# Kernel tuning notes

Hardware: AMD Instinct MI355X
Metric: run time of the kernel (lower is better)

## Reference

```python
import jax, jax.numpy as jnp
import numpy as np

EPS = 1e-05

def _rms_norm(x, w, eps=EPS):
    xf = x.astype(jnp.float32)
    var = jnp.mean(xf * xf, axis=-1, keepdims=True)
    return (x * jax.lax.rsqrt(var + eps)) * w

def _apply_rotary_emb(x, freqs_cis):
    # x: [B,S,H,D], freqs_cis: [B,S,D] with cos in first half, sin in second
    half = freqs_cis.shape[-1] // 2
    cos = freqs_cis[..., :half][:, :, None, :]  # [B,S,1,D/2]
    sin = freqs_cis[..., half:][:, :, None, :]
    xf = x.astype(jnp.float32).reshape(*x.shape[:-1], -1, 2)
    xr, xi = xf[..., 0], xf[..., 1]
    out_r = xr * cos - xi * sin
    out_i = xr * sin + xi * cos
    out = jnp.stack([out_r, out_i], axis=-1).reshape(x.shape)
    return out.astype(x.dtype)

def setup_inputs() -> dict:
    key = jax.random.key(0)
    ks = jax.random.split(key, 8)
    B, S, D, H = 2, 4096, 2048, 16
    hd = D // H
    scale = 1.0 / np.sqrt(D)
    x = jax.random.normal(ks[0], (B, S, D), dtype=jnp.float32)
    freqs_cis = jax.random.normal(ks[1], (B, S, hd), dtype=jnp.float32)
    wq = jax.random.normal(ks[2], (D, D), dtype=jnp.float32) * scale
    wk = jax.random.normal(ks[3], (D, D), dtype=jnp.float32) * scale
    wv = jax.random.normal(ks[4], (D, D), dtype=jnp.float32) * scale
    wo = jax.random.normal(ks[5], (D, D), dtype=jnp.float32) * scale
    norm_q_w = jnp.ones((hd,), dtype=jnp.float32)
    norm_k_w = jnp.ones((hd,), dtype=jnp.float32)
    return {"x": x, "freqs_cis": freqs_cis, "wq": wq, "wk": wk, "wv": wv,
            "wo": wo, "norm_q_w": norm_q_w, "norm_k_w": norm_k_w}

def reference(x, freqs_cis, wq, wk, wv, wo, norm_q_w, norm_k_w):
    B, S, D = x.shape
    H = 16
    hd = D // H
    # Linear with torch convention: y = x @ W^T
    q = (x @ wq.T).reshape(B, S, H, hd)
    k = (x @ wk.T).reshape(B, S, H, hd)
    v = (x @ wv.T).reshape(B, S, H, hd)
    q = _rms_norm(q, norm_q_w)
    k = _rms_norm(k, norm_k_w)
    q = _apply_rotary_emb(q, freqs_cis)
    k = _apply_rotary_emb(k, freqs_cis)
    # SDPA: [B,H,S,hd]
    scale = 1.0 / jnp.sqrt(jnp.asarray(hd, dtype=jnp.float32))
    scores = jnp.einsum('bqhd,bkhd->bhqk', q, k) * scale
    attn = jax.nn.softmax(scores, axis=-1)
    out = jnp.einsum('bhqk,bkhd->bqhd', attn, v).reshape(B, S, D)
    return out @ wo.T
```

## Files before the change

kernel.cpp:

```cpp
#include <hip/hip_runtime.h>
#include <hip/hip_bf16.h>
#include <cstdint>
#include <cstdio>

typedef unsigned short ushort_t;
typedef __attribute__((ext_vector_type(8))) __bf16 bf16x8;
typedef __attribute__((ext_vector_type(2))) __bf16 bhalf2_t;
typedef __attribute__((ext_vector_type(8))) unsigned short us8;
typedef __attribute__((ext_vector_type(4))) unsigned short us4;
typedef __attribute__((ext_vector_type(4))) float f32x4;
typedef __attribute__((ext_vector_type(2))) float f32x2;

__device__ __forceinline__ ushort_t f2b(float f) {
  uint32_t u = __builtin_bit_cast(uint32_t, f);
  uint32_t r = (u + 0x7fffu + ((u >> 16) & 1u)) >> 16;
  return (ushort_t)r;
}
__device__ __forceinline__ float b2f(ushort_t s) {
  return __builtin_bit_cast(float, (uint32_t)s << 16);
}

__device__ __forceinline__ void gld_lds16(const void* g, void* l) {
  __builtin_amdgcn_global_load_lds(
      (__attribute__((address_space(1))) void*)(uintptr_t)g,
      (__attribute__((address_space(3))) void*)(uint32_t)(uintptr_t)l,
      16, 0, 0);
}

__global__ void cast_f2b(const float* __restrict__ src, ushort_t* __restrict__ dst, int n4) {
  int i = blockIdx.x * 256 + threadIdx.x;
  if (i < n4) {
    float4 f = ((const float4*)src)[i];
    us4 o = { f2b(f.x), f2b(f.y), f2b(f.z), f2b(f.w) };
    ((us4*)dst)[i] = o;
  }
}

__global__ void cast3_f2b(const float* __restrict__ a, const float* __restrict__ b,
                          const float* __restrict__ c, ushort_t* __restrict__ dst) {
  int i = blockIdx.x * 256 + threadIdx.x;
  int seg = i >> 20, local = i & 1048575;
  const float* src = (seg == 0) ? a : (seg == 1) ? b : c;
  float4 f = ((const float4*)src)[local];
  us4 o = { f2b(f.x), f2b(f.y), f2b(f.z), f2b(f.w) };
  ((us4*)dst)[i] = o;
}

template <typename OutT>
__global__ __launch_bounds__(256, 3) void gemm_bt(const ushort_t* __restrict__ A,
                                                  const ushort_t* __restrict__ B,
                                                  OutT* __restrict__ C,
                                                  int M, int N, int K) {
  __shared__ ushort_t As[128 * 64];
  __shared__ ushort_t Bs[128 * 64];
  const int w    = threadIdx.x >> 6;
  const int lane = threadIdx.x & 63;
  const int m_l  = lane & 15;
  const int quad = lane >> 4;
  const int m0 = blockIdx.y * 128, n0 = blockIdx.x * 128;
  const int wr = (w >> 1) * 64, wc = (w & 1) * 64;

  f32x4 acc[4][4];
#pragma unroll
  for (int i = 0; i < 4; ++i)
#pragma unroll
    for (int j = 0; j < 4; ++j) acc[i][j] = (f32x4){0.f, 0.f, 0.f, 0.f};

  const int lr = lane >> 3;
  const int sc8 = ((lane & 7) ^ lr) * 8;

  for (int k0 = 0; k0 < K; k0 += 64) {
#pragma unroll
    for (int t = 0; t < 4; ++t) {
      int ra = w * 32 + t * 8;
      gld_lds16(A + (size_t)(m0 + ra + lr) * K + k0 + sc8, &As[ra * 64]);
      gld_lds16(B + (size_t)(n0 + ra + lr) * K + k0 + sc8, &Bs[ra * 64]);
    }
    __syncthreads();
#pragma unroll
    for (int kk = 0; kk < 2; ++kk) {
      bf16x8 af[4], bf[4];
#pragma unroll
      for (int mt = 0; mt < 4; ++mt) {
        int row = wr + mt * 16 + m_l;
        af[mt] = __builtin_bit_cast(bf16x8,
            *(const us8*)&As[row * 64 + ((kk * 4 + quad) ^ (m_l & 7)) * 8]);
      }
#pragma unroll
      for (int nt = 0; nt < 4; ++nt) {
        int row = wc + nt * 16 + m_l;
        bf[nt] = __builtin_bit_cast(bf16x8,
            *(const us8*)&Bs[row * 64 + ((kk * 4 + quad) ^ (m_l & 7)) * 8]);
      }
#pragma unroll
      for (int mt = 0; mt < 4; ++mt)
#pragma unroll
        for (int nt = 0; nt < 4; ++nt)
          acc[mt][nt] = __builtin_amdgcn_mfma_f32_16x16x32_bf16(af[mt], bf[nt], acc[mt][nt], 0, 0, 0);
    }
    __syncthreads();
  }
#pragma unroll
  for (int mt = 0; mt < 4; ++mt)
#pragma unroll
    for (int nt = 0; nt < 4; ++nt)
#pragma unroll
      for (int r = 0; r < 4; ++r) {
        int row = m0 + wr + mt * 16 + quad * 4 + r;
        int col = n0 + wc + nt * 16 + m_l;
        float v = acc[mt][nt][r];
        if constexpr (__is_same(OutT, float)) C[(size_t)row * N + col] = v;
        else                                  C[(size_t)row * N + col] = f2b(v);
      }
}

__global__ void rmsrope(ushort_t* __restrict__ qkv, const float* __restrict__ freqs,
                        const float* __restrict__ wq, const float* __restrict__ wk) {
  int w = threadIdx.x >> 6, lane = threadIdx.x & 63;
  int rid = blockIdx.x * 4 + w;
  int h = rid & 15;
  int m = (rid >> 4) & 8191;
  int qk = rid >> 17;
  ushort_t* row = qkv + (size_t)m * 6144 + qk * 2048 + h * 128;
  uint32_t pr = *(const uint32_t*)(row + 2 * lane);
  float xr = b2f((ushort_t)(pr & 0xffff));
  float xi = b2f((ushort_t)(pr >> 16));
  float ss = xr * xr + xi * xi;
#pragma unroll
  for (int o = 1; o < 64; o <<= 1) ss += __shfl_xor(ss, o);
  float rinv = rsqrtf(ss * (1.f / 128.f) + 1e-5f);
  const float* wn = qk ? wk : wq;
  float nr = xr * rinv * wn[2 * lane];
  float ni = xi * rinv * wn[2 * lane + 1];
  float fc = freqs[(size_t)m * 128 + lane];
  float fs = freqs[(size_t)m * 128 + 64 + lane];
  float orr = nr * fc - ni * fs;
  float oii = nr * fs + ni * fc;
  const float k1 = 0.08838834764831845f * 1.4426950408889634f;
  float fscale = (qk == 0) ? k1 : 1.0f;
  orr *= fscale;
  oii *= fscale;
  *(uint32_t*)(row + 2 * lane) = (uint32_t)f2b(orr) | ((uint32_t)f2b(oii) << 16);
}

__global__ void transpose_v(const ushort_t* __restrict__ qkv, ushort_t* __restrict__ vt) {
  __shared__ ushort_t tile[64][136];
  int bh = blockIdx.y, s0 = blockIdx.x * 64;
  int b = bh >> 4, h = bh & 15;
  const ushort_t* src = qkv + (size_t)(b * 4096 + s0) * 6144 + 4096 + h * 128;
  int t = threadIdx.x;
  int r = t >> 2, c0 = (t & 3) * 32;
#pragma unroll
  for (int j = 0; j < 4; ++j)
    *(us8*)&tile[r][c0 + 8 * j] = *(const us8*)(src + (size_t)r * 6144 + c0 + 8 * j);
  __syncthreads();
  int d = t >> 1, sh = (t & 1) * 32;
  ushort_t* dst = vt + (size_t)bh * 524288 + (size_t)d * 4096 + s0 + sh;
#pragma unroll
  for (int i0 = 0; i0 < 32; i0 += 8) {
    us8 o;
#pragma unroll
    for (int j = 0; j < 8; ++j) o[j] = tile[sh + i0 + j][d];
    *(us8*)(dst + i0) = o;
  }
}

__global__ __launch_bounds__(256, 3) void flash_attn(const ushort_t* __restrict__ qkv,
                                                     const ushort_t* __restrict__ vt,
                                                     ushort_t* __restrict__ op0,
                                                     ushort_t* __restrict__ op1,
                                                     ushort_t* __restrict__ op2,
                                                     ushort_t* __restrict__ lbase) {
  __shared__ ushort_t Ks[64 * 128];
  __shared__ ushort_t VTs[128 * 64];

  const int w = threadIdx.x >> 6, lane = threadIdx.x & 63;
  const int m_l = lane & 15, quad = lane >> 4;

  const int id = blockIdx.x;
  const int xcd = id & 7, j = id >> 3;
  const int combo = xcd * 12 + (j >> 5);
  const int q0 = (j & 31) * 128;
  const int bh = combo & 31, split = combo >> 5;
  const int b = bh >> 4, h = bh & 15;
  const int kvbeg = split * 1344;
  const int kvend = (split == 2) ? 4096 : kvbeg + 1344;
  ushort_t* op = (split == 0) ? op0 : (split == 1) ? op1 : op2;

  const ushort_t* qb = qkv + (size_t)(b * 4096 + q0) * 6144 + h * 128;
  const ushort_t* kb = qkv + (size_t)(b * 4096) * 6144 + 2048 + h * 128;
  const ushort_t* vb = vt + (size_t)bh * 524288;

  const int lr = lane >> 4, p15 = lane & 15;

  bf16x8 qf[2][4];
  const int rowq = w * 16 + m_l;
  const int sqr = (m_l & 3) | ((m_l >> 3) << 2) | ((w & 1) << 3);
#pragma unroll
  for (int g = 0; g < 2; ++g) {
    __syncthreads();
#pragma unroll
    for (int t = 0; t < 4; ++t) {
      int rbase = w * 16 + t * 4;
      int sst = lr | ((t >> 1) << 2) | ((w & 1) << 3);
      gld_lds16(qb + (size_t)(g * 64 + rbase + lr) * 6144 + (p15 ^ sst) * 8, &Ks[rbase * 128]);
    }
    __syncthreads();
#pragma unroll
    for (int kk = 0; kk < 4; ++kk)
      qf[g][kk] = __builtin_bit_cast(bf16x8,
          *(const us8*)&Ks[rowq * 128 + ((kk * 4 + quad) ^ sqr) * 8]);
  }

  int kbase[4];
#pragma unroll
  for (int mt = 0; mt < 4; ++mt)
    kbase[mt] = ((m_l >> 2) * 8 + (m_l & 3) + (mt & 1) * 4 + (mt >> 1) * 32) * 128;
  int cx[4];
#pragma unroll
  for (int kk = 0; kk < 4; ++kk) cx[kk] = ((kk * 4 + quad) ^ m_l) * 8;
  int vx[2];
#pragma unroll
  for (int kk = 0; kk < 2; ++kk) vx[kk] = ((kk * 4 + quad) ^ (m_l & 7)) * 8;

  f32x4 lacc[2] = {(f32x4){0.f, 0.f, 0.f, 0.f}, (f32x4){0.f, 0.f, 0.f, 0.f}};
  f32x4 Oa[2][8];
#pragma unroll
  for (int g = 0; g < 2; ++g)
#pragma unroll
    for (int nt = 0; nt < 8; ++nt) Oa[g][nt] = (f32x4){0.f, 0.f, 0.f, 0.f};

  for (int kv0 = kvbeg; kv0 < kvend; kv0 += 64) {
    __syncthreads();
    {
#pragma unroll
      for (int t = 0; t < 4; ++t) {
        int rbase = w * 16 + t * 4;
        int sst = lr | ((t >> 1) << 2) | ((w & 1) << 3);
        gld_lds16(kb + (size_t)(kv0 + rbase + lr) * 6144 + (p15 ^ sst) * 8, &Ks[rbase * 128]);
      }
      int lr2 = lane >> 3, s2 = (lane & 7) ^ lr2;
#pragma unroll
      for (int t = 0; t < 4; ++t) {
        int r = w * 32 + t * 8;
        gld_lds16(vb + (size_t)(r + lr2) * 4096 + kv0 + s2 * 8, &VTs[r * 64]);
      }
    }
    __syncthreads();

    f32x4 S[2][4];
#pragma unroll
    for (int g = 0; g < 2; ++g)
#pragma unroll
      for (int mt = 0; mt < 4; ++mt) S[g][mt] = (f32x4){0.f, 0.f, 0.f, 0.f};
#pragma unroll
    for (int kk = 0; kk < 4; ++kk)
#pragma unroll
      for (int mt = 0; mt < 4; ++mt) {
        bf16x8 kf = __builtin_bit_cast(bf16x8, *(const us8*)&Ks[kbase[mt] + cx[kk]]);
        S[0][mt] = __builtin_amdgcn_mfma_f32_16x16x32_bf16(kf, qf[0][kk], S[0][mt], 0, 0, 0);
        S[1][mt] = __builtin_amdgcn_mfma_f32_16x16x32_bf16(kf, qf[1][kk], S[1][mt], 0, 0, 0);
      }

    union Upf { us8 u; bhalf2_t h[4]; } pf[2][2];
#pragma unroll
    for (int g = 0; g < 2; ++g) {
      f32x4 pe[4];
#pragma unroll
      for (int mt = 0; mt < 4; ++mt)
#pragma unroll
        for (int r = 0; r < 4; ++r)
          pe[mt][r] = __builtin_amdgcn_exp2f(S[g][mt][r]);
      lacc[g] += (pe[0] + pe[1]) + (pe[2] + pe[3]);
#pragma unroll
      for (int kk = 0; kk < 2; ++kk)
#pragma unroll
        for (int t = 0; t < 4; ++t) {
          int mt = kk * 2 + (t >> 1), r0 = (t & 1) * 2;
          f32x2 a = { pe[mt][r0], pe[mt][r0 + 1] };
          pf[g][kk].h[t] = __builtin_convertvector(a, bhalf2_t);
        }
    }

#pragma unroll
    for (int kk = 0; kk < 2; ++kk) {
      bf16x8 p0 = __builtin_bit_cast(bf16x8, pf[0][kk].u);
      bf16x8 p1 = __builtin_bit_cast(bf16x8, pf[1][kk].u);
#pragma unroll
      for (int nt = 0; nt < 8; ++nt) {
        bf16x8 vf = __builtin_bit_cast(bf16x8,
            *(const us8*)&VTs[(nt * 16 + m_l) * 64 + vx[kk]]);
        Oa[0][nt] = __builtin_amdgcn_mfma_f32_16x16x32_bf16(p0, vf, Oa[0][nt], 0, 0, 0);
        Oa[1][nt] = __builtin_amdgcn_mfma_f32_16x16x32_bf16(p1, vf, Oa[1][nt], 0, 0, 0);
      }
    }
  }

#pragma unroll
  for (int g = 0; g < 2; ++g) {
    float lsum = (lacc[g][0] + lacc[g][1]) + (lacc[g][2] + lacc[g][3]);
    lsum += __shfl_xor(lsum, 16);
    lsum += __shfl_xor(lsum, 32);
    if (quad == 0) {
      int s = q0 + g * 64 + w * 16 + m_l;
      *(float*)(lbase + (size_t)(b * 4096 + s) * 6144 + 4096 + h * 128 + split * 2) = lsum;
    }
#pragma unroll
    for (int r = 0; r < 4; ++r) {
      int s = q0 + g * 64 + w * 16 + quad * 4 + r;
      ushort_t* dst = op + (size_t)(b * 4096 + s) * 2048 + h * 128;
#pragma unroll
      for (int nt = 0; nt < 8; ++nt) dst[nt * 16 + m_l] = f2b(Oa[g][nt][r]);
    }
  }
}

__global__ void combine_splits(ushort_t* __restrict__ p0, const ushort_t* __restrict__ p1,
                               const ushort_t* __restrict__ p2, const ushort_t* __restrict__ lbase) {
  int tid = blockIdx.x * 256 + threadIdx.x;
  int row = tid >> 4;
  int brow = row >> 4, h = row & 15;
  const float* lp = (const float*)(lbase + (size_t)brow * 6144 + 4096 + h * 128);
  float inv = 1.f / (lp[0] + lp[1] + lp[2]);
  size_t off = (size_t)tid * 8;
  us8 a = *(const us8*)(p0 + off);
  us8 bb = *(const us8*)(p1 + off);
  us8 c = *(const us8*)(p2 + off);
  us8 o;
#pragma unroll
  for (int i = 0; i < 8; ++i)
    o[i] = f2b((b2f(a[i]) + b2f(bb[i]) + b2f(c[i])) * inv);
  *(us8*)(p0 + off) = o;
}

extern "C" void kernel_launch(void* const* d_in, const int* in_sizes, int n_in,
                              void* d_out, int out_size, void* d_ws, size_t ws_size,
                              hipStream_t stream) {
  const float* x     = (const float*)d_in[0];
  const float* freqs = (const float*)d_in[1];
  const float* wq    = (const float*)d_in[2];
  const float* wk    = (const float*)d_in[3];
  const float* wv    = (const float*)d_in[4];
  const float* wo    = (const float*)d_in[5];
  const float* nqw   = (const float*)d_in[6];
  const float* nkw   = (const float*)d_in[7];
  float* out = (float*)d_out;

  char* ws = (char*)d_ws;
  ushort_t* xb    = (ushort_t*)(ws);
  ushort_t* wqkvb = (ushort_t*)(ws + 33554432);
  ushort_t* qkvb  = (ushort_t*)(ws + 67108864);
  ushort_t* vtb   = (ushort_t*)(ws + 167772160);
  ushort_t* ctxb  = (ushort_t*)(ws + 201326592);
  ushort_t* part2 = wqkvb;
  ushort_t* wob2  = xb;
  if (ws_size < 234881024) { fprintf(stderr, "kernel_launch: ws too small (%zu < 234881024)\n", ws_size); return; }

  cast_f2b<<<16384, 256, 0, stream>>>(x, xb, 4194304);
  cast3_f2b<<<12288, 256, 0, stream>>>(wq, wk, wv, wqkvb);

  gemm_bt<ushort_t><<<dim3(48, 64), 256, 0, stream>>>(xb, wqkvb, qkvb, 8192, 6144, 2048);
  rmsrope<<<65536, 256, 0, stream>>>(qkvb, freqs, nqw, nkw);
  transpose_v<<<dim3(64, 32), 256, 0, stream>>>(qkvb, vtb);
  flash_attn<<<3072, 256, 0, stream>>>(qkvb, vtb, ctxb, xb, part2, qkvb);
  combine_splits<<<8192, 256, 0, stream>>>(ctxb, xb, part2, qkvb);
  cast_f2b<<<4096, 256, 0, stream>>>(wo, wob2, 1048576);
  gemm_bt<float><<<dim3(16, 64), 256, 0, stream>>>(ctxb, wob2, out, 8192, 2048, 2048);
}
```

Measured before the change: 825.5 us.

## Enlarge GEMM tiles to 256x256 with double-buffered LDS and MFMA priority hints

The GEMM moves from 128x128 tiles with 4 waves to 256x256 tiles with 8 waves. LDS is double-buffered so the next K tile's global-to-LDS loads are issued before computing the current one, which removes one barrier per iteration. s_setprio hints are wrapped around the MFMA clusters in both the GEMM and the flash attention loops. The aim is more data reuse per tile and overlap of loads with compute. The cost is 128KB of LDS, higher register pressure, and fewer blocks for the output-projection GEMM (256 blocks on a many-CU device), which can leave compute units idle.

```diff
diff --git a/kernel.cpp b/kernel.cpp
--- a/kernel.cpp
+++ b/kernel.cpp
@@ -47,61 +47,85 @@
 }
 
 template <typename OutT>
-__global__ __launch_bounds__(256, 3) void gemm_bt(const ushort_t* __restrict__ A,
+__global__ __launch_bounds__(512, 2) void gemm_bt(const ushort_t* __restrict__ A,
                                                   const ushort_t* __restrict__ B,
                                                   OutT* __restrict__ C,
                                                   int M, int N, int K) {
-  __shared__ ushort_t As[128 * 64];
-  __shared__ ushort_t Bs[128 * 64];
+  __shared__ ushort_t As0[256 * 64], As1[256 * 64];
+  __shared__ ushort_t Bs0[256 * 64], Bs1[256 * 64];
   const int w    = threadIdx.x >> 6;
   const int lane = threadIdx.x & 63;
   const int m_l  = lane & 15;
   const int quad = lane >> 4;
-  const int m0 = blockIdx.y * 128, n0 = blockIdx.x * 128;
-  const int wr = (w >> 1) * 64, wc = (w & 1) * 64;
-
-  f32x4 acc[4][4];
-#pragma unroll
-  for (int i = 0; i < 4; ++i)
+  const int m0 = blockIdx.y * 256, n0 = blockIdx.x * 256;
+  const int wr = (w >> 2) * 128, wc = (w & 3) * 64;
+
+  f32x4 acc[8][4];
+#pragma unroll
+  for (int i = 0; i < 8; ++i)
 #pragma unroll
     for (int j = 0; j < 4; ++j) acc[i][j] = (f32x4){0.f, 0.f, 0.f, 0.f};
 
   const int lr = lane >> 3;
   const int sc8 = ((lane & 7) ^ lr) * 8;
-
-  for (int k0 = 0; k0 < K; k0 += 64) {
-#pragma unroll
-    for (int t = 0; t < 4; ++t) {
-      int ra = w * 32 + t * 8;
-      gld_lds16(A + (size_t)(m0 + ra + lr) * K + k0 + sc8, &As[ra * 64]);
-      gld_lds16(B + (size_t)(n0 + ra + lr) * K + k0 + sc8, &Bs[ra * 64]);
-    }
-    __syncthreads();
-#pragma unroll
-    for (int kk = 0; kk < 2; ++kk) {
-      bf16x8 af[4], bf[4];
-#pragma unroll
-      for (int mt = 0; mt < 4; ++mt) {
-        int row = wr + mt * 16 + m_l;
-        af[mt] = __builtin_bit_cast(bf16x8,
-            *(const us8*)&As[row * 64 + ((kk * 4 + quad) ^ (m_l & 7)) * 8]);
-      }
-#pragma unroll
-      for (int nt = 0; nt < 4; ++nt) {
-        int row = wc + nt * 16 + m_l;
-        bf[nt] = __builtin_bit_cast(bf16x8,
-            *(const us8*)&Bs[row * 64 + ((kk * 4 + quad) ^ (m_l & 7)) * 8]);
-      }
-#pragma unroll
-      for (int mt = 0; mt < 4; ++mt)
-#pragma unroll
-        for (int nt = 0; nt < 4; ++nt)
-          acc[mt][nt] = __builtin_amdgcn_mfma_f32_16x16x32_bf16(af[mt], bf[nt], acc[mt][nt], 0, 0, 0);
-    }
-    __syncthreads();
-  }
-#pragma unroll
-  for (int mt = 0; mt < 4; ++mt)
+  const int ra = w * 32;
+  const ushort_t* Ab = A + (size_t)(m0 + ra + lr) * K + sc8;
+  const ushort_t* Bb = B + (size_t)(n0 + ra + lr) * K + sc8;
+
+#pragma unroll
+  for (int t = 0; t < 4; ++t) {
+    gld_lds16(Ab + (size_t)(t * 8) * K, &As0[(ra + t * 8) * 64]);
+    gld_lds16(Bb + (size_t)(t * 8) * K, &Bs0[(ra + t * 8) * 64]);
+  }
+  __syncthreads();
+
+  const int ntile = K >> 6;
+
+  auto tile = [&](const ushort_t* Asc, const ushort_t* Bsc,
+                  ushort_t* Asn, ushort_t* Bsn, int ti) {
+    if (ti + 1 < ntile) {
+      const size_t kn = (size_t)(ti + 1) * 64;
+#pragma unroll
+      for (int t = 0; t < 4; ++t) {
+        gld_lds16(Ab + (size_t)(t * 8) * K + kn, &Asn[(ra + t * 8) * 64]);
+        gld_lds16(Bb + (size_t)(t * 8) * K + kn, &Bsn[(ra + t * 8) * 64]);
+      }
+    }
+#pragma unroll
+    for (int ph = 0; ph < 4; ++ph) {
+      const int mh = ph >> 1, nh = ph & 1;
+#pragma unroll
+      for (int kk = 0; kk < 2; ++kk) {
+        bf16x8 af[4], bg[2];
+        const int cx = ((kk * 4 + quad) ^ (m_l & 7)) * 8;
+#pragma unroll
+        for (int mt = 0; mt < 4; ++mt)
+          af[mt] = __builtin_bit_cast(bf16x8,
+              *(const us8*)&Asc[(wr + (mh * 4 + mt) * 16 + m_l) * 64 + cx]);
+#pragma unroll
+        for (int nt = 0; nt < 2; ++nt)
+          bg[nt] = __builtin_bit_cast(bf16x8,
+              *(const us8*)&Bsc[(wc + (nh * 2 + nt) * 16 + m_l) * 64 + cx]);
+        __builtin_amdgcn_s_setprio(1);
+#pragma unroll
+        for (int mt = 0; mt < 4; ++mt)
+#pragma unroll
+          for (int nt = 0; nt < 2; ++nt)
+            acc[mh * 4 + mt][nh * 2 + nt] = __builtin_amdgcn_mfma_f32_16x16x32_bf16(
+                af[mt], bg[nt], acc[mh * 4 + mt][nh * 2 + nt], 0, 0, 0);
+        __builtin_amdgcn_s_setprio(0);
+      }
+    }
+    __syncthreads();
+  };
+
+  for (int ti = 0; ti < ntile; ti += 2) {
+    tile(As0, Bs0, As1, Bs1, ti);
+    tile(As1, Bs1, As0, Bs0, ti + 1);
+  }
+
+#pragma unroll
+  for (int mt = 0; mt < 8; ++mt)
 #pragma unroll
     for (int nt = 0; nt < 4; ++nt)
 #pragma unroll
@@ -253,6 +277,7 @@
     for (int g = 0; g < 2; ++g)
 #pragma unroll
       for (int mt = 0; mt < 4; ++mt) S[g][mt] = (f32x4){0.f, 0.f, 0.f, 0.f};
+    __builtin_amdgcn_s_setprio(1);
 #pragma unroll
     for (int kk = 0; kk < 4; ++kk)
 #pragma unroll
@@ -261,6 +286,7 @@
         S[0][mt] = __builtin_amdgcn_mfma_f32_16x16x32_bf16(kf, qf[0][kk], S[0][mt], 0, 0, 0);
         S[1][mt] = __builtin_amdgcn_mfma_f32_16x16x32_bf16(kf, qf[1][kk], S[1][mt], 0, 0, 0);
       }
+    __builtin_amdgcn_s_setprio(0);
 
     union Upf { us8 u; bhalf2_t h[4]; } pf[2][2];
 #pragma unroll
@@ -282,6 +308,7 @@
         }
     }
 
+    __builtin_amdgcn_s_setprio(1);
 #pragma unroll
     for (int kk = 0; kk < 2; ++kk) {
       bf16x8 p0 = __builtin_bit_cast(bf16x8, pf[0][kk].u);
@@ -294,6 +321,7 @@
         Oa[1][nt] = __builtin_amdgcn_mfma_f32_16x16x32_bf16(p1, vf, Oa[1][nt], 0, 0, 0);
       }
     }
+    __builtin_amdgcn_s_setprio(0);
   }
 
 #pragma unroll
@@ -359,11 +387,11 @@
   cast_f2b<<<16384, 256, 0, stream>>>(x, xb, 4194304);
   cast3_f2b<<<12288, 256, 0, stream>>>(wq, wk, wv, wqkvb);
 
-  gemm_bt<ushort_t><<<dim3(48, 64), 256, 0, stream>>>(xb, wqkvb, qkvb, 8192, 6144, 2048);
+  gemm_bt<ushort_t><<<dim3(24, 32), 512, 0, stream>>>(xb, wqkvb, qkvb, 8192, 6144, 2048);
   rmsrope<<<65536, 256, 0, stream>>>(qkvb, freqs, nqw, nkw);
   transpose_v<<<dim3(64, 32), 256, 0, stream>>>(qkvb, vtb);
   flash_attn<<<3072, 256, 0, stream>>>(qkvb, vtb, ctxb, xb, part2, qkvb);
   combine_splits<<<8192, 256, 0, stream>>>(ctxb, xb, part2, qkvb);
   cast_f2b<<<4096, 256, 0, stream>>>(wo, wob2, 1048576);
-  gemm_bt<float><<<dim3(16, 64), 256, 0, stream>>>(ctxb, wob2, out, 8192, 2048, 2048);
-}
+  gemm_bt<float><<<dim3(8, 32), 512, 0, stream>>>(ctxb, wob2, out, 8192, 2048, 2048);
+}
```

New measurement: 784.6 us. 5.0% less time.
